# Kernel optimization log

Hardware: AMD Instinct MI355X
Metric: run time of the kernel (lower is better)

Reference implementation:

```python
import jax, jax.numpy as jnp
import numpy as np

M_FIELDS = 26   # cin_size[0]
H1 = 128        # cin_size[1]
H2 = 128        # cin_size[2]
BATCH = 2048
EMB_K = 32


def setup_inputs() -> dict:
    key = jax.random.key(0)
    k0, k1, k2, k3, k4 = jax.random.split(key, 5)
    inputs = jax.random.normal(k0, (BATCH, M_FIELDS, EMB_K), dtype=jnp.float32)
    # Conv3d(1, H1, kernel=(26,26,1)) -> weight [H1, H_prev=26, m=26], bias [H1]
    W1 = jax.random.normal(k1, (H1, M_FIELDS, M_FIELDS), dtype=jnp.float32) * 0.05
    b1 = jax.random.normal(k2, (H1,), dtype=jnp.float32) * 0.05
    # Conv3d(1, H2, kernel=(H1,26,1)) -> weight [H2, H1, m=26], bias [H2]
    W2 = jax.random.normal(k3, (H2, H1, M_FIELDS), dtype=jnp.float32) * 0.05
    b2 = jax.random.normal(k4, (H2,), dtype=jnp.float32) * 0.05
    return {"inputs": inputs, "W1": W1, "b1": b1, "W2": W2, "b2": b2}


def _cin_layer(x_prev, x0, W, b):
    # x_prev: [B, H_prev, k], x0: [B, m, k], W: [H, H_prev, m], b: [H]
    # Equivalent to: outer product z[b,i,j,k] = x_prev[b,i,k]*x0[b,j,k],
    # then Conv3d with kernel (H_prev, m, 1): out[b,h,k] = sum_ij W[h,i,j]*z + b[h]
    return jnp.einsum('bik,bjk,hij->bhk', x_prev, x0, W) + b[None, :, None]


def reference(inputs, W1, b1, W2, b2):
    x1 = _cin_layer(inputs, inputs, W1, b1)   # [B, H1, k]
    x2 = _cin_layer(x1, inputs, W2, b2)       # [B, H2, k]
    res = jnp.concatenate([x1, x2], axis=1)   # [B, H1+H2, k]
    return jnp.sum(res, axis=-1)              # [B, H1+H2]
```

## Files before the change

kernel.cpp:

```cpp
#include <hip/hip_runtime.h>

typedef __bf16 bf16;
typedef __bf16 bf16x8 __attribute__((ext_vector_type(8)));
typedef __bf16 bf16x4 __attribute__((ext_vector_type(4)));
typedef float f32x4 __attribute__((ext_vector_type(4)));
typedef unsigned int u32;

#define NB    2048
#define NM    26
#define NJP   27

__global__ __launch_bounds__(256) void prep_all(
    const float* __restrict__ W1, const float* __restrict__ W2,
    bf16* __restrict__ w1t, bf16* __restrict__ w2t2)
{
  const int bid = blockIdx.x, t = threadIdx.x;
  #pragma unroll
  for (int g = 0; g < 4; ++g) {
    int ge = g*160768 + bid*256 + t;
    if (ge < 110592) {
      int e = ge;
      int el = e & 7, lr = (e >> 3) & 15, lq = (e >> 7) & 3, ni = (e >> 9) & 3;
      int rest = e >> 11;
      int c = rest % NJP, cs_idx = rest / NJP;
      int h = cs_idx*64 + ni*16 + lr;
      int i = lq*8 + el;
      float v = (i < NM && c < NM) ? W1[h*(NM*NM) + i*NM + c] : 0.f;
      w1t[e] = (bf16)v;
    } else {
      int e = ge - 110592;
      int el = e & 7, lr = (e >> 3) & 15, lq = (e >> 7) & 3, ni = (e >> 9) & 3;
      int rest = e >> 11;
      int kc = rest % 130, cs_idx = rest / 130;
      int h = cs_idx*64 + ni*16 + lr;
      int c = lq*8 + el;
      float v = (kc < 128 && c < NM) ? W2[h*(128*NM) + kc*NM + c] : 0.f;
      w2t2[e] = (bf16)v;
    }
  }
}

#define STEP(CUR, NXT, J) do {                                                 \
  { int jn = ((J)+1 > 25) ? 25 : (J)+1;         \
    scf[NXT][0][0] = spw0[jn*32];  scf[NXT][0][1] = spw0[jn*32 + 16];          \
    scf[NXT][1][0] = spw1[jn*32];  scf[NXT][1][1] = spw1[jn*32 + 16]; }        \
  _Pragma("unroll")                                                            \
  for (int ni = 0; ni < 4; ++ni)                                               \
    B[NXT][ni] = *(const bf16x8*)(tb + (long)((J)+1)*2048 + ni*512);           \
  _Pragma("unroll")                                                            \
  for (int bb = 0; bb < 2; ++bb)                                               \
    _Pragma("unroll")                                                          \
    for (int mi = 0; mi < 2; ++mi) {                                           \
      bf16x8 af;                                                               \
      _Pragma("unroll")                                                        \
      for (int e = 0; e < 8; ++e)                                              \
        af[e] = (bf16)(xf32[bb][mi][e] * scf[CUR][bb][mi]);                    \
      _Pragma("unroll")                                                        \
      for (int ni = 0; ni < 4; ++ni)                                           \
        acc[bb][mi][ni] = __builtin_amdgcn_mfma_f32_16x16x32_bf16(af,          \
                                    B[CUR][ni], acc[bb][mi][ni], 0, 0, 0);     \
    }                                                                          \
} while (0)

#define STEPM(CA, NA, KL, Q) do {                                              \
  Af[NA] = *(const bf16x8*)&ldsU[(((KL)+1)*4 + lq)*72 + lr*8];                 \
  Bf[((Q)+3)&3][0] = *(const bf16x8*)(Bb0 + (long)((KL)+3)*2048);              \
  Bf[((Q)+3)&3][1] = *(const bf16x8*)(Bb1 + (long)((KL)+3)*2048);              \
  _Pragma("unroll")                                                            \
  for (int ht = 0; ht < 2; ++ht)                                               \
    acc2[ht] = __builtin_amdgcn_mfma_f32_16x16x32_bf16(Af[CA], Bf[(Q)][ht],    \
                                                       acc2[ht], 0, 0, 0);     \
} while (0)

__global__ __launch_bounds__(256, 3) void cinfuse(
    const float* __restrict__ in, const bf16* __restrict__ w1t,
    const bf16* __restrict__ w2t2, const float* __restrict__ b1,
    const float* __restrict__ b2, float* __restrict__ out)
{
  __shared__ __align__(16) bf16 ldsU[264*72];
  const int t = threadIdx.x, bid = blockIdx.x;
  const int lane = t & 63, w = t >> 6;
  const int lr = lane & 15, lq = lane >> 4;
  const int fo = lq*128 + lr*8;
  const int cs_idx = bid & 1, cs = cs_idx * 64;
  const int grp = bid >> 1;
  const int bw0 = grp*8 + w*2;

  const float* bin0 = in + (long)bw0*(NM*32);
  const float* bin1 = bin0 + NM*32;
  const float* spw0 = bin0 + lr;
  const float* spw1 = bin1 + lr;

  float xf32[2][2][8];
  #pragma unroll
  for (int bb = 0; bb < 2; ++bb) {
    const float* bin = bb ? bin1 : bin0;
    #pragma unroll
    for (int mi = 0; mi < 2; ++mi)
      #pragma unroll
      for (int e = 0; e < 8; ++e) {
        int j = lq*8 + e;
        xf32[bb][mi][e] = (j < NM) ? bin[j*32 + mi*16 + lr] : 0.f;
      }
  }

  f32x4 acc[2][2][4];
  #pragma unroll
  for (int bb=0; bb<2; ++bb)
    #pragma unroll
    for (int mi=0; mi<2; ++mi)
      #pragma unroll
      for (int ni=0; ni<4; ++ni) acc[bb][mi][ni] = {0.f,0.f,0.f,0.f};

  const bf16* tb = w1t + (long)cs_idx*NJP*2048 + fo;

  float scf[2][2][2];
  bf16x8 B[2][4];
  #pragma unroll
  for (int ni = 0; ni < 4; ++ni)
    B[0][ni] = *(const bf16x8*)(tb + ni*512);
  scf[0][0][0] = spw0[0];  scf[0][0][1] = spw0[16];
  scf[0][1][0] = spw1[0];  scf[0][1][1] = spw1[16];

  for (int jj = 0; jj < 13; ++jj) {
    STEP(0, 1, 2*jj);
    STEP(1, 0, 2*jj + 1);
  }

  float bias[4];
  #pragma unroll
  for (int ni=0; ni<4; ++ni) bias[ni] = b1[cs + ni*16 + lr];

  bf16* T = &ldsU[w*2304];

  bf16x8 agr[2][4];
  bf16x8 bgr[2][2];

  #pragma unroll
  for (int bb = 0; bb < 2; ++bb) {
    const int bw = bw0 + bb;
    const float* bin = bb ? bin1 : bin0;

    #pragma unroll
    for (int ni=0; ni<4; ++ni) {
      float vv = 0.f;
      #pragma unroll
      for (int mi=0; mi<2; ++mi)
        #pragma unroll
        for (int r=0; r<4; ++r) vv += acc[bb][mi][ni][r];
      vv += __shfl_xor(vv, 16, 64);
      vv += __shfl_xor(vv, 32, 64);
      if (lq == 0) out[bw*256 + cs + ni*16 + lr] = vv + 32.0f * bias[ni];
    }

    #pragma unroll
    for (int mi=0; mi<2; ++mi)
      #pragma unroll
      for (int ni=0; ni<4; ++ni) {
        bf16x4 pk;
        #pragma unroll
        for (int r=0; r<4; ++r) pk[r] = (bf16)(acc[bb][mi][ni][r] + bias[ni]);
        *(bf16x4*)&T[(ni*16+lr)*36 + mi*16 + lq*4] = pk;
      }

    #pragma unroll
    for (int mt = 0; mt < 4; ++mt)
      agr[bb][mt] = *(const bf16x8*)&T[(mt*16+lr)*36 + lq*8];

    #pragma unroll
    for (int nt = 0; nt < 2; ++nt) {
      int j = nt*16 + lr;
      bf16x8 vv;
      #pragma unroll
      for (int e=0; e<8; ++e) vv[e] = (bf16)0.f;
      if (j < NM) {
        const float* src = bin + j*32 + lq*8;
        f32x4 a = *(const f32x4*)src, c = *(const f32x4*)(src+4);
        #pragma unroll
        for (int e=0; e<4; ++e) { vv[e] = (bf16)a[e]; vv[4+e] = (bf16)c[e]; }
      }
      bgr[bb][nt] = vv;
    }
  }

  __syncthreads();

  #pragma unroll
  for (int bb = 0; bb < 2; ++bb) {
    const int bloc = w*2 + bb;
    #pragma unroll
    for (int mt = 0; mt < 4; ++mt) {
      #pragma unroll
      for (int nt = 0; nt < 2; ++nt) {
        f32x4 z = {0.f,0.f,0.f,0.f};
        f32x4 g = __builtin_amdgcn_mfma_f32_16x16x32_bf16(bgr[bb][nt],
                                                          agr[bb][mt], z, 0, 0, 0);
        bf16x4 pk;
        #pragma unroll
        for (int r = 0; r < 4; ++r) pk[r] = (bf16)g[r];
        const int kh = (mt*16 + lr)*4 + nt*2 + (lq >> 1);
        *(bf16x4*)&ldsU[kh*72 + bloc*8 + (lq & 1)*4] = pk;
      }
    }
  }

  __syncthreads();

  const int ht0 = w*2, ht1 = w*2 + 1;
  const bf16* Bb0 = w2t2 + ((long)(ht0 >> 2)*130 + cs)*2048 + (ht0 & 3)*512 + fo;
  const bf16* Bb1 = w2t2 + ((long)(ht1 >> 2)*130 + cs)*2048 + (ht1 & 3)*512 + fo;

  f32x4 acc2[2];
  acc2[0] = {0.f,0.f,0.f,0.f};  acc2[1] = {0.f,0.f,0.f,0.f};

  bf16x8 Af[2], Bf[4][2];
  Af[0] = *(const bf16x8*)&ldsU[lq*72 + lr*8];
  #pragma unroll
  for (int d = 0; d < 3; ++d) {
    Bf[d][0] = *(const bf16x8*)(Bb0 + (long)d*2048);
    Bf[d][1] = *(const bf16x8*)(Bb1 + (long)d*2048);
  }

  for (int jj = 0; jj < 16; ++jj) {
    const int KL0 = jj*4;
    STEPM(0, 1, KL0+0, 0);
    STEPM(1, 0, KL0+1, 1);
    STEPM(0, 1, KL0+2, 2);
    STEPM(1, 0, KL0+3, 3);
  }

  if (cs_idx == 0) {
    #pragma unroll
    for (int ht = 0; ht < 2; ++ht) {
      float bv = 32.0f * b2[(w*2 + ht)*16 + lr];
      #pragma unroll
      for (int r=0; r<4; ++r) acc2[ht][r] += bv;
    }
  }

  if (lq < 2) {
    #pragma unroll
    for (int ht = 0; ht < 2; ++ht) {
      int h = (w*2 + ht)*16 + lr;
      #pragma unroll
      for (int r=0; r<4; ++r) {
        int b = grp*8 + lq*4 + r;
        atomicAdd(&out[b*256 + 128 + h], acc2[ht][r]);
      }
    }
  }
}

extern "C" void kernel_launch(void* const* d_in, const int* in_sizes, int n_in,
                              void* d_out, int out_size, void* d_ws, size_t ws_size,
                              hipStream_t stream) {
  const float* in = (const float*)d_in[0];
  const float* W1 = (const float*)d_in[1];
  const float* b1 = (const float*)d_in[2];
  const float* W2 = (const float*)d_in[3];
  const float* b2 = (const float*)d_in[4];
  float* out = (float*)d_out;

  char* ws = (char*)d_ws;
  bf16* w1t  = (bf16*)(ws);
  bf16* w2t2 = (bf16*)(ws + 1048576);

  prep_all<<<628, 256, 0, stream>>>(W1, W2, w1t, w2t2);
  cinfuse <<<512, 256, 0, stream>>>(in, w1t, w2t2, b1, b2, out);
}
```

Measured before the change: 92.57 us.

## Split hidden dimension four ways across blocks, halving per-block work and LDS

The kernel now splits the 128 first-layer output channels into four 32-wide slices instead of two 64-wide slices. This doubles the grid to 1024 blocks, halves the LDS footprint, and raises the occupancy hint to 4 blocks per CU. The outer-product MFMA for layer 2 now runs before the barrier and is kept in registers. The split trades better occupancy and parallelism for more redundant input loads and twice as many atomic adds into the layer-2 outputs.

New measurement: 97.60 us. 5.4% more time.

```diff
diff --git a/kernel.cpp b/kernel.cpp
--- a/kernel.cpp
+++ b/kernel.cpp
@@ -12,7 +12,7 @@
 
 __global__ __launch_bounds__(256) void prep_all(
     const float* __restrict__ W1, const float* __restrict__ W2,
-    bf16* __restrict__ w1t, bf16* __restrict__ w2t2)
+    bf16* __restrict__ w1q, bf16* __restrict__ w2t2)
 {
   const int bid = blockIdx.x, t = threadIdx.x;
   #pragma unroll
@@ -20,13 +20,13 @@
     int ge = g*160768 + bid*256 + t;
     if (ge < 110592) {
       int e = ge;
-      int el = e & 7, lr = (e >> 3) & 15, lq = (e >> 7) & 3, ni = (e >> 9) & 3;
-      int rest = e >> 11;
-      int c = rest % NJP, cs_idx = rest / NJP;
-      int h = cs_idx*64 + ni*16 + lr;
+      int el = e & 7, lr = (e >> 3) & 15, lq = (e >> 7) & 3, ni = (e >> 9) & 1;
+      int rest = e >> 10;
+      int c = rest % NJP, q = rest / NJP;
+      int h = q*32 + ni*16 + lr;
       int i = lq*8 + el;
       float v = (i < NM && c < NM) ? W1[h*(NM*NM) + i*NM + c] : 0.f;
-      w1t[e] = (bf16)v;
+      w1q[e] = (bf16)v;
     } else {
       int e = ge - 110592;
       int el = e & 7, lr = (e >> 3) & 15, lq = (e >> 7) & 3, ni = (e >> 9) & 3;
@@ -45,8 +45,8 @@
     scf[NXT][0][0] = spw0[jn*32];  scf[NXT][0][1] = spw0[jn*32 + 16];          \
     scf[NXT][1][0] = spw1[jn*32];  scf[NXT][1][1] = spw1[jn*32 + 16]; }        \
   _Pragma("unroll")                                                            \
-  for (int ni = 0; ni < 4; ++ni)                                               \
-    B[NXT][ni] = *(const bf16x8*)(tb + (long)((J)+1)*2048 + ni*512);           \
+  for (int ni = 0; ni < 2; ++ni)                                               \
+    B[NXT][ni] = *(const bf16x8*)(tb + (long)((J)+1)*1024 + ni*512);           \
   _Pragma("unroll")                                                            \
   for (int bb = 0; bb < 2; ++bb)                                               \
     _Pragma("unroll")                                                          \
@@ -56,7 +56,7 @@
       for (int e = 0; e < 8; ++e)                                              \
         af[e] = (bf16)(xf32[bb][mi][e] * scf[CUR][bb][mi]);                    \
       _Pragma("unroll")                                                        \
-      for (int ni = 0; ni < 4; ++ni)                                           \
+      for (int ni = 0; ni < 2; ++ni)                                           \
         acc[bb][mi][ni] = __builtin_amdgcn_mfma_f32_16x16x32_bf16(af,          \
                                     B[CUR][ni], acc[bb][mi][ni], 0, 0, 0);     \
     }                                                                          \
@@ -72,18 +72,18 @@
                                                        acc2[ht], 0, 0, 0);     \
 } while (0)
 
-__global__ __launch_bounds__(256, 3) void cinfuse(
-    const float* __restrict__ in, const bf16* __restrict__ w1t,
+__global__ __launch_bounds__(256, 4) void cinfuse(
+    const float* __restrict__ in, const bf16* __restrict__ w1q,
     const bf16* __restrict__ w2t2, const float* __restrict__ b1,
     const float* __restrict__ b2, float* __restrict__ out)
 {
-  __shared__ __align__(16) bf16 ldsU[264*72];
+  __shared__ __align__(16) bf16 ldsU[136*72];
   const int t = threadIdx.x, bid = blockIdx.x;
   const int lane = t & 63, w = t >> 6;
   const int lr = lane & 15, lq = lane >> 4;
   const int fo = lq*128 + lr*8;
-  const int cs_idx = bid & 1, cs = cs_idx * 64;
-  const int grp = bid >> 1;
+  const int q = bid & 3, h0 = q*32;
+  const int grp = bid >> 2;
   const int bw0 = grp*8 + w*2;
 
   const float* bin0 = in + (long)bw0*(NM*32);
@@ -104,20 +104,20 @@
       }
   }
 
-  f32x4 acc[2][2][4];
+  f32x4 acc[2][2][2];
   #pragma unroll
   for (int bb=0; bb<2; ++bb)
     #pragma unroll
     for (int mi=0; mi<2; ++mi)
       #pragma unroll
-      for (int ni=0; ni<4; ++ni) acc[bb][mi][ni] = {0.f,0.f,0.f,0.f};
-
-  const bf16* tb = w1t + (long)cs_idx*NJP*2048 + fo;
+      for (int ni=0; ni<2; ++ni) acc[bb][mi][ni] = {0.f,0.f,0.f,0.f};
+
+  const bf16* tb = w1q + (long)q*NJP*1024 + fo;
 
   float scf[2][2][2];
-  bf16x8 B[2][4];
-  #pragma unroll
-  for (int ni = 0; ni < 4; ++ni)
+  bf16x8 B[2][2];
+  #pragma unroll
+  for (int ni = 0; ni < 2; ++ni)
     B[0][ni] = *(const bf16x8*)(tb + ni*512);
   scf[0][0][0] = spw0[0];  scf[0][0][1] = spw0[16];
   scf[0][1][0] = spw1[0];  scf[0][1][1] = spw1[16];
@@ -127,14 +127,13 @@
     STEP(1, 0, 2*jj + 1);
   }
 
-  float bias[4];
-  #pragma unroll
-  for (int ni=0; ni<4; ++ni) bias[ni] = b1[cs + ni*16 + lr];
-
-  bf16* T = &ldsU[w*2304];
-
-  bf16x8 agr[2][4];
-  bf16x8 bgr[2][2];
+  float bias[2];
+  #pragma unroll
+  for (int ni=0; ni<2; ++ni) bias[ni] = b1[h0 + ni*16 + lr];
+
+  bf16* T = &ldsU[w*1152];
+
+  bf16x4 pk[2][2][2];
 
   #pragma unroll
   for (int bb = 0; bb < 2; ++bb) {
@@ -142,7 +141,7 @@
     const float* bin = bb ? bin1 : bin0;
 
     #pragma unroll
-    for (int ni=0; ni<4; ++ni) {
+    for (int ni=0; ni<2; ++ni) {
       float vv = 0.f;
       #pragma unroll
       for (int mi=0; mi<2; ++mi)
@@ -150,23 +149,20 @@
         for (int r=0; r<4; ++r) vv += acc[bb][mi][ni][r];
       vv += __shfl_xor(vv, 16, 64);
       vv += __shfl_xor(vv, 32, 64);
-      if (lq == 0) out[bw*256 + cs + ni*16 + lr] = vv + 32.0f * bias[ni];
+      if (lq == 0) out[bw*256 + h0 + ni*16 + lr] = vv + 32.0f * bias[ni];
     }
 
     #pragma unroll
     for (int mi=0; mi<2; ++mi)
       #pragma unroll
-      for (int ni=0; ni<4; ++ni) {
-        bf16x4 pk;
-        #pragma unroll
-        for (int r=0; r<4; ++r) pk[r] = (bf16)(acc[bb][mi][ni][r] + bias[ni]);
-        *(bf16x4*)&T[(ni*16+lr)*36 + mi*16 + lq*4] = pk;
-      }
-
-    #pragma unroll
-    for (int mt = 0; mt < 4; ++mt)
-      agr[bb][mt] = *(const bf16x8*)&T[(mt*16+lr)*36 + lq*8];
-
+      for (int ni=0; ni<2; ++ni) {
+        bf16x4 p;
+        #pragma unroll
+        for (int r=0; r<4; ++r) p[r] = (bf16)(acc[bb][mi][ni][r] + bias[ni]);
+        *(bf16x4*)&T[(ni*16+lr)*36 + mi*16 + lq*4] = p;
+      }
+
+    bf16x8 bg[2];
     #pragma unroll
     for (int nt = 0; nt < 2; ++nt) {
       int j = nt*16 + lr;
@@ -179,7 +175,18 @@
         #pragma unroll
         for (int e=0; e<4; ++e) { vv[e] = (bf16)a[e]; vv[4+e] = (bf16)c[e]; }
       }
-      bgr[bb][nt] = vv;
+      bg[nt] = vv;
+    }
+    #pragma unroll
+    for (int mt = 0; mt < 2; ++mt) {
+      bf16x8 ag = *(const bf16x8*)&T[(mt*16+lr)*36 + lq*8];
+      #pragma unroll
+      for (int nt = 0; nt < 2; ++nt) {
+        f32x4 z = {0.f,0.f,0.f,0.f};
+        f32x4 g = __builtin_amdgcn_mfma_f32_16x16x32_bf16(bg[nt], ag, z, 0, 0, 0);
+        #pragma unroll
+        for (int r = 0; r < 4; ++r) pk[bb][mt][nt][r] = (bf16)g[r];
+      }
     }
   }
 
@@ -189,26 +196,19 @@
   for (int bb = 0; bb < 2; ++bb) {
     const int bloc = w*2 + bb;
     #pragma unroll
-    for (int mt = 0; mt < 4; ++mt) {
+    for (int mt = 0; mt < 2; ++mt)
       #pragma unroll
       for (int nt = 0; nt < 2; ++nt) {
-        f32x4 z = {0.f,0.f,0.f,0.f};
-        f32x4 g = __builtin_amdgcn_mfma_f32_16x16x32_bf16(bgr[bb][nt],
-                                                          agr[bb][mt], z, 0, 0, 0);
-        bf16x4 pk;
-        #pragma unroll
-        for (int r = 0; r < 4; ++r) pk[r] = (bf16)g[r];
         const int kh = (mt*16 + lr)*4 + nt*2 + (lq >> 1);
-        *(bf16x4*)&ldsU[kh*72 + bloc*8 + (lq & 1)*4] = pk;
-      }
-    }
+        *(bf16x4*)&ldsU[kh*72 + bloc*8 + (lq & 1)*4] = pk[bb][mt][nt];
+      }
   }
 
   __syncthreads();
 
   const int ht0 = w*2, ht1 = w*2 + 1;
-  const bf16* Bb0 = w2t2 + ((long)(ht0 >> 2)*130 + cs)*2048 + (ht0 & 3)*512 + fo;
-  const bf16* Bb1 = w2t2 + ((long)(ht1 >> 2)*130 + cs)*2048 + (ht1 & 3)*512 + fo;
+  const bf16* Bb0 = w2t2 + ((long)(ht0 >> 2)*130 + q*32)*2048 + (ht0 & 3)*512 + fo;
+  const bf16* Bb1 = w2t2 + ((long)(ht1 >> 2)*130 + q*32)*2048 + (ht1 & 3)*512 + fo;
 
   f32x4 acc2[2];
   acc2[0] = {0.f,0.f,0.f,0.f};  acc2[1] = {0.f,0.f,0.f,0.f};
@@ -221,7 +221,7 @@
     Bf[d][1] = *(const bf16x8*)(Bb1 + (long)d*2048);
   }
 
-  for (int jj = 0; jj < 16; ++jj) {
+  for (int jj = 0; jj < 8; ++jj) {
     const int KL0 = jj*4;
     STEPM(0, 1, KL0+0, 0);
     STEPM(1, 0, KL0+1, 1);
@@ -229,7 +229,7 @@
     STEPM(1, 0, KL0+3, 3);
   }
 
-  if (cs_idx == 0) {
+  if (q == 0) {
     #pragma unroll
     for (int ht = 0; ht < 2; ++ht) {
       float bv = 32.0f * b2[(w*2 + ht)*16 + lr];
@@ -262,9 +262,9 @@
   float* out = (float*)d_out;
 
   char* ws = (char*)d_ws;
-  bf16* w1t  = (bf16*)(ws);
+  bf16* w1q  = (bf16*)(ws);
   bf16* w2t2 = (bf16*)(ws + 1048576);
 
-  prep_all<<<628, 256, 0, stream>>>(W1, W2, w1t, w2t2);
-  cinfuse <<<512, 256, 0, stream>>>(in, w1t, w2t2, b1, b2, out);
+  prep_all<<<628,  256, 0, stream>>>(W1, W2, w1q, w2t2);
+  cinfuse <<<1024, 256, 0, stream>>>(in, w1q, w2t2, b1, b2, out);
 }
```
